# Kernel tuning notes

Hardware: AMD Instinct MI355X
Metric: run time of the kernel (lower is better)

## Reference

```python
import jax, jax.numpy as jnp
import numpy as np

IN_CH, OUT_CH, B, H, W = 32, 64, 8, 256, 256
EPS = 1e-5

SOBEL_X = [[1., 0., -1.], [2., 0., -2.], [1., 0., -1.]]
SOBEL_Y = [[1., 2., 1.], [0., 0., 0.], [-1., -2., -1.]]
LAP = [[0., 1., 0.], [1., -4., 1.], [0., 1., 0.]]

DN = ('NCHW', 'OIHW', 'NCHW')


def conv2d(x, w, b, pad, groups=1):
    y = jax.lax.conv_general_dilated(x, w, (1, 1), [(pad, pad), (pad, pad)],
                                     dimension_numbers=DN, feature_group_count=groups)
    return y + b[None, :, None, None]


def dw_conv(x, k2d):
    # fixed depthwise 3x3 conv, groups=C, padding=1, no bias
    c = x.shape[1]
    kern = jnp.tile(jnp.asarray(k2d, x.dtype)[None, None], (c, 1, 1, 1))  # (C,1,3,3)
    return jax.lax.conv_general_dilated(x, kern, (1, 1), [(1, 1), (1, 1)],
                                        dimension_numbers=DN, feature_group_count=c)


def bn4d(x, p):  # eval-mode BN; x (B,C,H,W), p (4,C) = gamma, beta, mean, var
    g, b, m, v = p
    s = g * jax.lax.rsqrt(v + EPS)
    return (x - m[None, :, None, None]) * s[None, :, None, None] + b[None, :, None, None]


def bn2d(h, p):  # h (B,C)
    g, b, m, v = p
    return (h - m) * (g * jax.lax.rsqrt(v + EPS)) + b


def _bn_params(key, c):
    k1, k2, k3, k4 = jax.random.split(key, 4)
    g = 1.0 + 0.1 * jax.random.normal(k1, (c,), jnp.float32)
    b = 0.1 * jax.random.normal(k2, (c,), jnp.float32)
    m = 0.1 * jax.random.normal(k3, (c,), jnp.float32)
    v = jax.random.uniform(k4, (c,), jnp.float32, 0.5, 1.5)
    return jnp.stack([g, b, m, v])


def setup_inputs() -> dict:
    key = jax.random.key(0)
    ks = jax.random.split(key, 24)
    s = 0.05
    return {
        'x': jax.random.normal(ks[0], (B, IN_CH, H, W), jnp.float32),
        'gate_w1': s * jax.random.normal(ks[1], (IN_CH, IN_CH), jnp.float32),
        'gate_b1': s * jax.random.normal(ks[2], (IN_CH,), jnp.float32),
        'gate_bn': _bn_params(ks[3], IN_CH),
        'gate_w2': s * jax.random.normal(ks[4], (3, IN_CH), jnp.float32),
        'gate_b2': s * jax.random.normal(ks[5], (3,), jnp.float32),
        'mw1': s * jax.random.normal(ks[6], (OUT_CH, IN_CH, 3, 3), jnp.float32),
        'mb1': s * jax.random.normal(ks[7], (OUT_CH,), jnp.float32),
        'mbn1': _bn_params(ks[8], OUT_CH),
        'mw2': s * jax.random.normal(ks[9], (OUT_CH, OUT_CH, 5, 5), jnp.float32),
        'mb2': s * jax.random.normal(ks[10], (OUT_CH,), jnp.float32),
        'mbn2': _bn_params(ks[11], OUT_CH),
        'sxw': s * jax.random.normal(ks[12], (OUT_CH, IN_CH, 5, 5), jnp.float32),
        'sxb': s * jax.random.normal(ks[13], (OUT_CH,), jnp.float32),
        'sxbn': _bn_params(ks[14], OUT_CH),
        'syw': s * jax.random.normal(ks[15], (OUT_CH, IN_CH, 5, 5), jnp.float32),
        'syb': s * jax.random.normal(ks[16], (OUT_CH,), jnp.float32),
        'sybn': _bn_params(ks[17], OUT_CH),
        'lw': s * jax.random.normal(ks[18], (OUT_CH, IN_CH, 5, 5), jnp.float32),
        'lb': s * jax.random.normal(ks[19], (OUT_CH,), jnp.float32),
        'lbn': _bn_params(ks[20], OUT_CH),
    }


def reference(x, gate_w1, gate_b1, gate_bn, gate_w2, gate_b2,
              mw1, mb1, mbn1, mw2, mb2, mbn2,
              sxw, sxb, sxbn, syw, syb, sybn, lw, lb, lbn):
    # gate: GAP -> 1x1 conv -> BN -> tanh -> 1x1 conv -> top-1 one-hot over 3 experts
    gap = x.mean((2, 3))                                   # (B, C_in)
    h = jnp.tanh(bn2d(gap @ gate_w1.T + gate_b1, gate_bn))
    k = h @ gate_w2.T + gate_b2                            # (B, 3)
    oh = jax.nn.one_hot(jnp.argmax(k, axis=1), 3, dtype=x.dtype)  # (B, 3)

    # expert 0: main branch (conv3x3+BN+ReLU -> conv5x5+BN+ReLU)
    main = jax.nn.relu(bn4d(conv2d(x, mw1, mb1, 1), mbn1))
    main = jax.nn.relu(bn4d(conv2d(main, mw2, mb2, 2), mbn2))

    # expert 1: mean of sobel-x and sobel-y branches
    sx = jax.nn.relu(bn4d(conv2d(dw_conv(x, SOBEL_X), sxw, sxb, 2), sxbn))
    sy = jax.nn.relu(bn4d(conv2d(dw_conv(x, SOBEL_Y), syw, syb, 2), sybn))
    sobel = (sx + sy) * 0.5

    # expert 2: laplacian branch
    lap = jax.nn.relu(bn4d(conv2d(dw_conv(x, LAP), lw, lb, 2), lbn))

    # one-hot gated combination (== stack + one_hot mask + sum in the original)
    w = oh[:, :, None, None, None]  # (B, 3, 1, 1, 1)
    return main * w[:, 0] + sobel * w[:, 1] + lap * w[:, 2]
```

## Files before the change

### kernel.cpp

```cpp
#include <hip/hip_runtime.h>

#define BB 8
#define IC 32
#define OC 64
#define HH 256
#define WW 256
#define EPS 1e-5f

typedef __attribute__((ext_vector_type(8))) short bf16x8;
typedef __attribute__((ext_vector_type(4))) float f32x4;

#define YSTR 40
#define XSTR 40

#define WS_GAP   0
#define WS_BIDX  256
#define WS_W1F   264
#define WS_B1F   (WS_W1F + 9216)
#define WS_W2F   (WS_B1F + 64)
#define WS_B2F   (WS_W2F + 51200)
#define WS_SXWT  (WS_B2F + 64)
#define WS_SXBF  (WS_SXWT + 51200)
#define WS_SYWT  (WS_SXBF + 64)
#define WS_SYBF  (WS_SYWT + 51200)
#define WS_LWT   (WS_SYBF + 64)
#define WS_LBF   (WS_LWT + 51200)
#define WS_XT    (WS_LBF + 64)
#define WS_ZPAD  (WS_XT + 8388608)
#define WS_NEED_FAST ((size_t)(WS_ZPAD + 16) * 4)

__device__ inline unsigned short bf16r(float f) {
    unsigned int u = __float_as_uint(f);
    unsigned int r = (u + 0x7fffu + ((u >> 16) & 1u)) >> 16;
    return (unsigned short)r;
}
__device__ inline float bf2f(unsigned short s) {
    return __uint_as_float(((unsigned int)s) << 16);
}

__device__ __forceinline__ void gld16(const void* g, const void* l) {
    __builtin_amdgcn_global_load_lds(
        (const __attribute__((address_space(1))) void*)(unsigned long long)(g),
        (__attribute__((address_space(3))) void*)(unsigned int)(unsigned long long)(l),
        16, 0, 0);
}

__global__ void prep_kernel(const float* __restrict__ mw1, const float* __restrict__ mb1, const float* __restrict__ mbn1,
                            const float* __restrict__ mw2, const float* __restrict__ mb2, const float* __restrict__ mbn2,
                            const float* __restrict__ sxw, const float* __restrict__ sxb, const float* __restrict__ sxbn,
                            const float* __restrict__ syw, const float* __restrict__ syb, const float* __restrict__ sybn,
                            const float* __restrict__ lw,  const float* __restrict__ lb,  const float* __restrict__ lbn,
                            float* __restrict__ ws, int fast) {
    int idx = blockIdx.x * 256 + threadIdx.x;

    if (idx < 18432) {
        int j = idx & 7, lane = (idx >> 3) & 63, oct = (idx >> 9) & 1, ht = idx >> 10;
        int t = ht % 9, h = ht / 9;
        int oc = h * 32 + oct * 16 + (lane & 15);
        int ic = (lane >> 4) * 8 + j;
        float s = mbn1[oc] * rsqrtf(mbn1[192 + oc] + EPS);
        ((unsigned short*)(ws + WS_W1F))[idx] = bf16r(mw1[(oc * IC + ic) * 9 + t] * s);
    }
    if (idx < 102400) {
        int j = idx & 7, lane = (idx >> 3) & 63, oct = (idx >> 9) & 3, ht = idx >> 11;
        int t = ht % 25, h = ht / 25;
        int oc = oct * 16 + (lane & 15);
        int ic = h * 32 + (lane >> 4) * 8 + j;
        float s = mbn2[oc] * rsqrtf(mbn2[192 + oc] + EPS);
        ((unsigned short*)(ws + WS_W2F))[idx] = bf16r(mw2[(oc * OC + ic) * 25 + t] * s);
    }
    if (idx < 51200) {
        int j = idx & 7, lane = (idx >> 3) & 63, oct = (idx >> 9) & 3, t = idx >> 11;
        int oc = oct * 16 + (lane & 15);
        int ic = (lane >> 4) * 8 + j;
        float ssx = sxbn[oc] * rsqrtf(sxbn[192 + oc] + EPS);
        float ssy = sybn[oc] * rsqrtf(sybn[192 + oc] + EPS);
        float sl  = lbn[oc]  * rsqrtf(lbn[192 + oc]  + EPS);
        ((unsigned short*)(ws + WS_SXWT))[idx] = bf16r(sxw[(oc * IC + ic) * 25 + t] * ssx);
        ((unsigned short*)(ws + WS_SYWT))[idx] = bf16r(syw[(oc * IC + ic) * 25 + t] * ssy);
        ((unsigned short*)(ws + WS_LWT ))[idx] = bf16r(lw [(oc * IC + ic) * 25 + t] * sl);
    }
    if (idx < 256) ws[WS_GAP + idx] = 0.f;
    if (fast && idx < 16) ws[WS_ZPAD + idx] = 0.f;
    if (idx < 64) {
        float s1 = mbn1[idx] * rsqrtf(mbn1[192 + idx] + EPS);
        ws[WS_B1F + idx] = (mb1[idx] - mbn1[128 + idx]) * s1 + mbn1[64 + idx];
        float s2 = mbn2[idx] * rsqrtf(mbn2[192 + idx] + EPS);
        ws[WS_B2F + idx] = (mb2[idx] - mbn2[128 + idx]) * s2 + mbn2[64 + idx];
        float sx = sxbn[idx] * rsqrtf(sxbn[192 + idx] + EPS);
        ws[WS_SXBF + idx] = (sxb[idx] - sxbn[128 + idx]) * sx + sxbn[64 + idx];
        float sy = sybn[idx] * rsqrtf(sybn[192 + idx] + EPS);
        ws[WS_SYBF + idx] = (syb[idx] - sybn[128 + idx]) * sy + sybn[64 + idx];
        float sl = lbn[idx] * rsqrtf(lbn[192 + idx] + EPS);
        ws[WS_LBF + idx] = (lb[idx] - lbn[128 + idx]) * sl + lbn[64 + idx];
    }
}

__global__ void __launch_bounds__(256, 2)
xform_kernel(const float* __restrict__ x, float* __restrict__ ws) {
    int b = blockIdx.y, row = blockIdx.x, t = threadIdx.x;
    const float* xb = x + (size_t)b * (IC * HH * WW) + (size_t)row * WW;

    unsigned int pk[16];
    #pragma unroll
    for (int k = 0; k < 32; k += 2) {
        float v0 = xb[(size_t)k * (HH * WW) + t];
        float v1 = xb[(size_t)(k + 1) * (HH * WW) + t];
        pk[k >> 1] = (unsigned int)bf16r(v0) | ((unsigned int)bf16r(v1) << 16);
    }
    short* xt = (short*)(ws + WS_XT) + ((size_t)b * (HH * WW) + (size_t)row * WW + t) * 32;
    uint4* dp = (uint4*)xt;
    dp[0] = make_uint4(pk[0],  pk[1],  pk[2],  pk[3]);
    dp[1] = make_uint4(pk[4],  pk[5],  pk[6],  pk[7]);
    dp[2] = make_uint4(pk[8],  pk[9],  pk[10], pk[11]);
    dp[3] = make_uint4(pk[12], pk[13], pk[14], pk[15]);

    __shared__ float gl[32];
    int w = t >> 6, lane = t & 63;
    #pragma unroll
    for (int kk = 0; kk < 8; kk++) {
        int k = w * 8 + kk;
        const float* rp = xb + (size_t)k * (HH * WW);
        float s = rp[lane] + rp[lane + 64] + rp[lane + 128] + rp[lane + 192];
        #pragma unroll
        for (int off = 32; off; off >>= 1) s += __shfl_down(s, off, 64);
        if (lane == 0) gl[k] = s;
    }
    __syncthreads();
    if (t < 32) atomicAdd(ws + WS_GAP + b * 32 + t, gl[t] * (1.f / (HH * WW)));
}

__global__ void gap_kernel(const float* __restrict__ x, float* __restrict__ ws) {
    int bc = blockIdx.x;
    const float4* p = (const float4*)(x + (size_t)bc * (HH * WW));
    float s = 0.f;
    for (int i = threadIdx.x; i < (HH * WW) / 4; i += 256) {
        float4 v = p[i];
        s += (v.x + v.y) + (v.z + v.w);
    }
    #pragma unroll
    for (int off = 32; off; off >>= 1) s += __shfl_down(s, off, 64);
    __shared__ float red[4];
    int lane = threadIdx.x & 63, w = threadIdx.x >> 6;
    if (lane == 0) red[w] = s;
    __syncthreads();
    if (threadIdx.x == 0)
        ws[WS_GAP + bc] = (red[0] + red[1] + red[2] + red[3]) * (1.f / (HH * WW));
}

__global__ void gate_kernel(const float* __restrict__ w1, const float* __restrict__ b1,
                            const float* __restrict__ gbn,
                            const float* __restrict__ w2, const float* __restrict__ b2,
                            float* __restrict__ ws) {
    __shared__ float hsh[8][32];
    int tid = threadIdx.x;
    int b = tid >> 5, j = tid & 31;
    float acc = b1[j];
    for (int i = 0; i < 32; i++) acc += ws[WS_GAP + b * 32 + i] * w1[j * 32 + i];
    float s = gbn[j] * rsqrtf(gbn[96 + j] + EPS);
    hsh[b][j] = tanhf((acc - gbn[64 + j]) * s + gbn[32 + j]);
    __syncthreads();
    if (tid < 8) {
        float best = -1e30f; int bi = 0;
        for (int c = 0; c < 3; c++) {
            float k = b2[c];
            for (int jj = 0; jj < 32; jj++) k += hsh[tid][jj] * w2[c * 32 + jj];
            if (k > best) { best = k; bi = c; }
        }
        ((int*)ws)[WS_BIDX + tid] = bi;
    }
}

template <int ASYNC>
__global__ void __launch_bounds__(256, 2)
main_kernel(const float* __restrict__ x, const float* __restrict__ ws, float* __restrict__ out) {
    __shared__ __align__(1024) short xs[ASYNC ? 496 * 32 : 484 * XSTR];
    __shared__ __align__(16)   short ys[400 * YSTR];

    int b = blockIdx.y;
    if (((const int*)ws)[WS_BIDX + b] != 0) return;
    int tile = blockIdx.x;
    int ty = (tile >> 4) * 16, tx = (tile & 15) * 16;
    int tid = threadIdx.x;
    int w = tid >> 6, lane = tid & 63, n = lane & 15, quad = lane >> 4;

    if constexpr (ASYNC) {
        const short* xtb = (const short*)(ws + WS_XT) + (size_t)b * (HH * WW * 32);
        const void* zp = (const void*)(ws + WS_ZPAD);
        for (int c = w; c < 31; c += 4) {
            int D = c * 1024 + (lane << 4);
            int L = D ^ (((D >> 7) & 7) << 4);
            int pL = L >> 6, qL = (L >> 4) & 3;
            int rr = pL / 22, cc2 = pL - rr * 22;
            int gy = ty - 3 + rr, gx = tx - 3 + cc2;
            bool v = (pL < 484) && ((unsigned)gy < HH) && ((unsigned)gx < WW);
            const void* src = v ? (const void*)(xtb + (((gy << 8) + gx) * 32) + (qL << 3)) : zp;
            gld16(src, (const void*)((const char*)xs + c * 1024));
        }
    } else {
        const float* xb = x + (size_t)b * IC * HH * WW;
        for (int p = tid; p < 484; p += 256) {
            int rr = p / 22, cc = p % 22;
            int gy = ty - 3 + rr, gx = tx - 3 + cc;
            bool v = ((unsigned)gy < HH) && ((unsigned)gx < WW);
            const float* xp = xb + gy * WW + gx;
            short* dst = xs + p * XSTR;
            #pragma unroll
            for (int ic = 0; ic < IC; ic += 4) {
                float f0 = v ? xp[(size_t)(ic + 0) * (HH * WW)] : 0.f;
                float f1 = v ? xp[(size_t)(ic + 1) * (HH * WW)] : 0.f;
                float f2 = v ? xp[(size_t)(ic + 2) * (HH * WW)] : 0.f;
                float f3 = v ? xp[(size_t)(ic + 3) * (HH * WW)] : 0.f;
                uint2 pk;
                pk.x = (unsigned int)bf16r(f0) | ((unsigned int)bf16r(f1) << 16);
                pk.y = (unsigned int)bf16r(f2) | ((unsigned int)bf16r(f3) << 16);
                *(uint2*)(dst + ic) = pk;
            }
        }
    }

    auto ldb = [&](int P) -> bf16x8 {
        if constexpr (ASYNC) {
            int L = (P << 6) + (quad << 4);
            int A = L ^ (((L >> 7) & 7) << 4);
            return *(const bf16x8*)((const char*)xs + A);
        } else {
            return *(const bf16x8*)(xs + P * XSTR + quad * 8);
        }
    };

    const short* w1v = (const short*)(ws + WS_W1F);
    const bf16x8* w2v = (const bf16x8*)(ws + WS_W2F);

    f32x4 acc2[4][4];
    #pragma unroll
    for (int i = 0; i < 4; i++)
        #pragma unroll
        for (int jj = 0; jj < 4; jj++) acc2[i][jj] = (f32x4){0.f, 0.f, 0.f, 0.f};
    int mrow0 = w * 4;
    int yr0   = w * 5;

    __syncthreads();

    #pragma unroll 1
    for (int h = 0; h < 2; h++) {
        if (h) __syncthreads();

        #pragma unroll
        for (int cg = 0; cg < 2; cg++) {
            int cb = cg * 4;
            f32x4 a1[5][2];
            #pragma unroll
            for (int rr = 0; rr < 5; rr++) {
                a1[rr][0] = (f32x4){0.f, 0.f, 0.f, 0.f};
                a1[rr][1] = (f32x4){0.f, 0.f, 0.f, 0.f};
            }
            #pragma unroll
            for (int dw = 0; dw < 3; dw++) {
                bf16x8 w1f[3][2];
                #pragma unroll
                for (int dh = 0; dh < 3; dh++) {
                    int t = dh * 3 + dw;
                    w1f[dh][0] = *(const bf16x8*)(w1v + (((h * 9 + t) * 2 + 0) * 64 + lane) * 8);
                    w1f[dh][1] = *(const bf16x8*)(w1v + (((h * 9 + t) * 2 + 1) * 64 + lane) * 8);
                }
                bf16x8 bfr[7];
                #pragma unroll
                for (int rI = 0; rI < 7; rI++)
                    bfr[rI] = ldb((yr0 + rI) * 22 + cb + n + dw);
                #pragma unroll
                for (int dh = 0; dh < 3; dh++)
                    #pragma unroll
                    for (int rr = 0; rr < 5; rr++) {
                        a1[rr][0] = __builtin_amdgcn_mfma_f32_16x16x32_bf16(w1f[dh][0], bfr[rr + dh], a1[rr][0], 0, 0, 0);
                        a1[rr][1] = __builtin_amdgcn_mfma_f32_16x16x32_bf16(w1f[dh][1], bfr[rr + dh], a1[rr][1], 0, 0, 0);
                    }
            }
            #pragma unroll
            for (int oct = 0; oct < 2; oct++) {
                float bias1[4];
                #pragma unroll
                for (int r = 0; r < 4; r++)
                    bias1[r] = ws[WS_B1F + h * 32 + oct * 16 + quad * 4 + r];
                #pragma unroll
                for (int rr = 0; rr < 5; rr++) {
                    int yr = yr0 + rr;
                    int gy2 = ty - 2 + yr, gx2 = tx - 2 + cb + n;
                    bool inb = ((unsigned)gy2 < HH) && ((unsigned)gx2 < WW);
                    float v0 = inb ? fmaxf(a1[rr][oct][0] + bias1[0], 0.f) : 0.f;
                    float v1 = inb ? fmaxf(a1[rr][oct][1] + bias1[1], 0.f) : 0.f;
                    float v2 = inb ? fmaxf(a1[rr][oct][2] + bias1[2], 0.f) : 0.f;
                    float v3 = inb ? fmaxf(a1[rr][oct][3] + bias1[3], 0.f) : 0.f;
                    uint2 pkk;
                    pkk.x = (unsigned int)bf16r(v0) | ((unsigned int)bf16r(v1) << 16);
                    pkk.y = (unsigned int)bf16r(v2) | ((unsigned int)bf16r(v3) << 16);
                    *(uint2*)(ys + (yr * 20 + cb + n) * YSTR + oct * 16 + quad * 4) = pkk;
                }
            }
        }
        __syncthreads();

        const bf16x8* w2h = w2v + (size_t)h * 100 * 64;
        bf16x8 afq[4][4];
        #pragma unroll
        for (int kp = 0; kp < 4; kp++) {
            int tn = (kp % 5) * 5 + (kp / 5);
            int base = tn * 256 + lane;
            afq[kp][0] = w2h[base];       afq[kp][1] = w2h[base + 64];
            afq[kp][2] = w2h[base + 128]; afq[kp][3] = w2h[base + 192];
        }
        bf16x8 bfr2[8];
        #pragma unroll
        for (int k = 0; k < 25; k++) {
            int dw = k / 5, dh = k % 5;
            if (dh == 0) {
                #pragma unroll
                for (int rI = 0; rI < 8; rI++)
                    bfr2[rI] = *(const bf16x8*)(ys + ((mrow0 + rI) * 20 + n + dw) * YSTR + quad * 8);
            }
            #pragma unroll
            for (int r4 = 0; r4 < 4; r4++) {
                bf16x8 bb = bfr2[r4 + dh];
                acc2[r4][0] = __builtin_amdgcn_mfma_f32_16x16x32_bf16(afq[k & 3][0], bb, acc2[r4][0], 0, 0, 0);
                acc2[r4][1] = __builtin_amdgcn_mfma_f32_16x16x32_bf16(afq[k & 3][1], bb, acc2[r4][1], 0, 0, 0);
                acc2[r4][2] = __builtin_amdgcn_mfma_f32_16x16x32_bf16(afq[k & 3][2], bb, acc2[r4][2], 0, 0, 0);
                acc2[r4][3] = __builtin_amdgcn_mfma_f32_16x16x32_bf16(afq[k & 3][3], bb, acc2[r4][3], 0, 0, 0);
            }
            if (k + 4 < 25) {
                int kk = k + 4;
                int tn = (kk % 5) * 5 + (kk / 5);
                int base = tn * 256 + lane;
                afq[k & 3][0] = w2h[base];       afq[k & 3][1] = w2h[base + 64];
                afq[k & 3][2] = w2h[base + 128]; afq[k & 3][3] = w2h[base + 192];
            }
        }
    }

    float bias2[4][4];
    #pragma unroll
    for (int oct = 0; oct < 4; oct++)
        #pragma unroll
        for (int r = 0; r < 4; r++)
            bias2[oct][r] = ws[WS_B2F + oct * 16 + quad * 4 + r];

    float* ob = out + (size_t)b * OC * HH * WW;
    #pragma unroll
    for (int r4 = 0; r4 < 4; r4++) {
        int orow = mrow0 + r4;
        #pragma unroll
        for (int oct = 0; oct < 4; oct++) {
            #pragma unroll
            for (int r = 0; r < 4; r++) {
                int oc = oct * 16 + quad * 4 + r;
                float v = fmaxf(acc2[r4][oct][r] + bias2[oct][r], 0.f);
                ob[(size_t)oc * (HH * WW) + (ty + orow) * WW + tx + n] = v;
            }
        }
    }
}

template <int ASYNC>
__global__ void __launch_bounds__(256, 2)
edge_kernel(const float* __restrict__ x, const float* __restrict__ ws, float* __restrict__ out) {
    constexpr float KSX[9] = {1, 0, -1, 2, 0, -2, 1, 0, -1};
    constexpr float KSY[9] = {1, 2, 1, 0, 0, 0, -1, -2, -1};
    constexpr float KLP[9] = {0, 1, 0, 1, -4, 1, 0, 1, 0};

    __shared__ __align__(1024) short xs[ASYNC ? 496 * 32 : 484 * XSTR];
    __shared__ __align__(16)   short ys[400 * YSTR];

    int b = blockIdx.y;
    int sel = ((const int*)ws)[WS_BIDX + b];
    if (sel == 0) return;
    int tile = blockIdx.x;
    int ty = (tile >> 4) * 16, tx = (tile & 15) * 16;
    int tid = threadIdx.x;
    int w = tid >> 6, lane = tid & 63, n = lane & 15, quad = lane >> 4;

    if constexpr (ASYNC) {
        const short* xtb = (const short*)(ws + WS_XT) + (size_t)b * (HH * WW * 32);
        const void* zp = (const void*)(ws + WS_ZPAD);
        for (int c = w; c < 31; c += 4) {
            int D = c * 1024 + (lane << 4);
            int L = D ^ (((D >> 7) & 7) << 4);
            int pL = L >> 6, qL = (L >> 4) & 3;
            int rr = pL / 22, cc2 = pL - rr * 22;
            int gy = ty - 3 + rr, gx = tx - 3 + cc2;
            bool v = (pL < 484) && ((unsigned)gy < HH) && ((unsigned)gx < WW);
            const void* src = v ? (const void*)(xtb + (((gy << 8) + gx) * 32) + (qL << 3)) : zp;
            gld16(src, (const void*)((const char*)xs + c * 1024));
        }
    } else {
        const float* xb = x + (size_t)b * IC * HH * WW;
        for (int p = tid; p < 484; p += 256) {
            int rr = p / 22, cc = p % 22;
            int gy = ty - 3 + rr, gx = tx - 3 + cc;
            bool v = ((unsigned)gy < HH) && ((unsigned)gx < WW);
            const float* xp = xb + gy * WW + gx;
            short* dst = xs + p * XSTR;
            #pragma unroll
            for (int ic = 0; ic < IC; ic += 4) {
                float f0 = v ? xp[(size_t)(ic + 0) * (HH * WW)] : 0.f;
                float f1 = v ? xp[(size_t)(ic + 1) * (HH * WW)] : 0.f;
                float f2 = v ? xp[(size_t)(ic + 2) * (HH * WW)] : 0.f;
                float f3 = v ? xp[(size_t)(ic + 3) * (HH * WW)] : 0.f;
                uint2 pk;
                pk.x = (unsigned int)bf16r(f0) | ((unsigned int)bf16r(f1) << 16);
                pk.y = (unsigned int)bf16r(f2) | ((unsigned int)bf16r(f3) << 16);
                *(uint2*)(dst + ic) = pk;
            }
        }
    }

    auto ldq = [&](int P, int q) -> bf16x8 {
        if constexpr (ASYNC) {
            int L = (P << 6) + (q << 4);
            int A = L ^ (((L >> 7) & 7) << 4);
            return *(const bf16x8*)((const char*)xs + A);
        } else {
            return *(const bf16x8*)(xs + P * XSTR + q * 8);
        }
    };

    int mrow0 = w * 4;
    int npass = (sel == 1) ? 2 : 1;
    f32x4 accA[4][4];
    f32x4 acc2[4][4];

    __syncthreads();

    #pragma unroll 1
    for (int pass = 0; pass < npass; pass++) {
        int kid = (sel == 1) ? pass : 2;
        if (pass) __syncthreads();

        for (int t2 = tid; t2 < 1600; t2 += 256) {
            int q = t2 & 3, px = t2 >> 2;
            int pr = px / 20, pc = px - pr * 20;
            bool inb = ((unsigned)(ty - 2 + pr) < HH) && ((unsigned)(tx - 2 + pc) < WW);
            float a[8] = {0.f, 0.f, 0.f, 0.f, 0.f, 0.f, 0.f, 0.f};
            if (inb) {
                #pragma unroll
                for (int dr = 0; dr < 3; dr++)
                    #pragma unroll
                    for (int dc = 0; dc < 3; dc++) {
                        float kv = (kid == 0) ? KSX[dr * 3 + dc]
                                 : (kid == 1) ? KSY[dr * 3 + dc]
                                              : KLP[dr * 3 + dc];
                        if (kv != 0.f) {
                            bf16x8 v = ldq((pr + dr) * 22 + pc + dc, q);
                            #pragma unroll
                            for (int j = 0; j < 8; j++)
                                a[j] += kv * bf2f((unsigned short)v[j]);
                        }
                    }
            }
            uint4 pk;
            pk.x = (unsigned int)bf16r(a[0]) | ((unsigned int)bf16r(a[1]) << 16);
            pk.y = (unsigned int)bf16r(a[2]) | ((unsigned int)bf16r(a[3]) << 16);
            pk.z = (unsigned int)bf16r(a[4]) | ((unsigned int)bf16r(a[5]) << 16);
            pk.w = (unsigned int)bf16r(a[6]) | ((unsigned int)bf16r(a[7]) << 16);
            *(uint4*)(ys + px * YSTR + q * 8) = pk;
        }
        __syncthreads();

        #pragma unroll
        for (int i = 0; i < 4; i++)
            #pragma unroll
            for (int jj = 0; jj < 4; jj++) acc2[i][jj] = (f32x4){0.f, 0.f, 0.f, 0.f};

        const bf16x8* wf = (const bf16x8*)(ws + (kid == 0 ? WS_SXWT : kid == 1 ? WS_SYWT : WS_LWT));
        bf16x8 afq[2][4];
        #pragma unroll
        for (int kp = 0; kp < 2; kp++) {
            int tn = kp * 5;
            int base = tn * 256 + lane;
            afq[kp][0] = wf[base];       afq[kp][1] = wf[base + 64];
            afq[kp][2] = wf[base + 128]; afq[kp][3] = wf[base + 192];
        }
        bf16x8 bfr2[8];
        #pragma unroll
        for (int k = 0; k < 25; k++) {
            int dw = k / 5, dh = k % 5;
            if (dh == 0) {
                #pragma unroll
                for (int rI = 0; rI < 8; rI++)
                    bfr2[rI] = *(const bf16x8*)(ys + ((mrow0 + rI) * 20 + n + dw) * YSTR + quad * 8);
            }
            #pragma unroll
            for (int r4 = 0; r4 < 4; r4++) {
                bf16x8 bb = bfr2[r4 + dh];
                acc2[r4][0] = __builtin_amdgcn_mfma_f32_16x16x32_bf16(afq[k & 1][0], bb, acc2[r4][0], 0, 0, 0);
                acc2[r4][1] = __builtin_amdgcn_mfma_f32_16x16x32_bf16(afq[k & 1][1], bb, acc2[r4][1], 0, 0, 0);
                acc2[r4][2] = __builtin_amdgcn_mfma_f32_16x16x32_bf16(afq[k & 1][2], bb, acc2[r4][2], 0, 0, 0);
                acc2[r4][3] = __builtin_amdgcn_mfma_f32_16x16x32_bf16(afq[k & 1][3], bb, acc2[r4][3], 0, 0, 0);
            }
            if (k + 2 < 25) {
                int kk = k + 2;
                int tn = (kk % 5) * 5 + (kk / 5);
                int base = tn * 256 + lane;
                afq[k & 1][0] = wf[base];       afq[k & 1][1] = wf[base + 64];
                afq[k & 1][2] = wf[base + 128]; afq[k & 1][3] = wf[base + 192];
            }
        }
        if (sel == 1 && pass == 0) {
            #pragma unroll
            for (int i = 0; i < 4; i++)
                #pragma unroll
                for (int jj = 0; jj < 4; jj++) accA[i][jj] = acc2[i][jj];
        }
    }

    float* ob = out + (size_t)b * OC * HH * WW;
    #pragma unroll
    for (int r4 = 0; r4 < 4; r4++) {
        int orow = mrow0 + r4;
        #pragma unroll
        for (int oct = 0; oct < 4; oct++) {
            #pragma unroll
            for (int r = 0; r < 4; r++) {
                int oc = oct * 16 + quad * 4 + r;
                float v;
                if (sel == 1) {
                    float vx = fmaxf(accA[r4][oct][r] + ws[WS_SXBF + oc], 0.f);
                    float vy = fmaxf(acc2[r4][oct][r] + ws[WS_SYBF + oc], 0.f);
                    v = 0.5f * (vx + vy);
                } else {
                    v = fmaxf(acc2[r4][oct][r] + ws[WS_LBF + oc], 0.f);
                }
                ob[(size_t)oc * (HH * WW) + (ty + orow) * WW + tx + n] = v;
            }
        }
    }
}

extern "C" void kernel_launch(void* const* d_in, const int* in_sizes, int n_in,
                              void* d_out, int out_size, void* d_ws, size_t ws_size,
                              hipStream_t stream) {
    const float* x    = (const float*)d_in[0];
    const float* gw1  = (const float*)d_in[1];
    const float* gb1  = (const float*)d_in[2];
    const float* gbn  = (const float*)d_in[3];
    const float* gw2  = (const float*)d_in[4];
    const float* gb2  = (const float*)d_in[5];
    const float* mw1  = (const float*)d_in[6];
    const float* mb1  = (const float*)d_in[7];
    const float* mbn1 = (const float*)d_in[8];
    const float* mw2  = (const float*)d_in[9];
    const float* mb2  = (const float*)d_in[10];
    const float* mbn2 = (const float*)d_in[11];
    const float* sxw  = (const float*)d_in[12];
    const float* sxb  = (const float*)d_in[13];
    const float* sxbn = (const float*)d_in[14];
    const float* syw  = (const float*)d_in[15];
    const float* syb  = (const float*)d_in[16];
    const float* sybn = (const float*)d_in[17];
    const float* lw   = (const float*)d_in[18];
    const float* lb   = (const float*)d_in[19];
    const float* lbn  = (const float*)d_in[20];
    float* ws  = (float*)d_ws;
    float* out = (float*)d_out;

    int fast = (ws_size >= WS_NEED_FAST) ? 1 : 0;

    prep_kernel<<<400, 256, 0, stream>>>(mw1, mb1, mbn1, mw2, mb2, mbn2,
                                         sxw, sxb, sxbn, syw, syb, sybn, lw, lb, lbn, ws, fast);
    if (fast) {
        xform_kernel<<<dim3(HH, BB), 256, 0, stream>>>(x, ws);
    } else {
        gap_kernel<<<256, 256, 0, stream>>>(x, ws);
    }
    gate_kernel<<<1, 256, 0, stream>>>(gw1, gb1, gbn, gw2, gb2, ws);

    dim3 grid(256, BB);
    if (fast) {
        main_kernel<1><<<grid, 256, 0, stream>>>(x, ws, out);
        edge_kernel<1><<<grid, 256, 0, stream>>>(x, ws, out);
    } else {
        main_kernel<0><<<grid, 256, 0, stream>>>(x, ws, out);
        edge_kernel<0><<<grid, 256, 0, stream>>>(x, ws, out);
    }
}
```

Baseline: 435.7 us.

## Pad transformed input with zero halo and read main-branch operands directly from global

```diff
diff --git a/kernel.cpp b/kernel.cpp
--- a/kernel.cpp
+++ b/kernel.cpp
@@ -6,6 +6,9 @@
 #define HH 256
 #define WW 256
 #define EPS 1e-5f
+
+#define XTW 264
+#define XTP (XTW * XTW)
 
 typedef __attribute__((ext_vector_type(8))) short bf16x8;
 typedef __attribute__((ext_vector_type(4))) float f32x4;
@@ -26,7 +29,8 @@
 #define WS_LWT   (WS_SYBF + 64)
 #define WS_LBF   (WS_LWT + 51200)
 #define WS_XT    (WS_LBF + 64)
-#define WS_ZPAD  (WS_XT + 8388608)
+#define WS_XT_U4 2230272
+#define WS_ZPAD  (WS_XT + 8921088)
 #define WS_NEED_FAST ((size_t)(WS_ZPAD + 16) * 4)
 
 __device__ inline unsigned short bf16r(float f) {
@@ -52,6 +56,9 @@
                             const float* __restrict__ lw,  const float* __restrict__ lb,  const float* __restrict__ lbn,
                             float* __restrict__ ws, int fast) {
     int idx = blockIdx.x * 256 + threadIdx.x;
+
+    if (fast && idx < WS_XT_U4)
+        ((uint4*)(ws + WS_XT))[idx] = make_uint4(0u, 0u, 0u, 0u);
 
     if (idx < 18432) {
         int j = idx & 7, lane = (idx >> 3) & 63, oct = (idx >> 9) & 1, ht = idx >> 10;
@@ -108,7 +115,7 @@
         float v1 = xb[(size_t)(k + 1) * (HH * WW) + t];
         pk[k >> 1] = (unsigned int)bf16r(v0) | ((unsigned int)bf16r(v1) << 16);
     }
-    short* xt = (short*)(ws + WS_XT) + ((size_t)b * (HH * WW) + (size_t)row * WW + t) * 32;
+    short* xt = (short*)(ws + WS_XT) + ((size_t)b * XTP + (size_t)(row + 3) * XTW + (t + 3)) * 32;
     uint4* dp = (uint4*)xt;
     dp[0] = make_uint4(pk[0],  pk[1],  pk[2],  pk[3]);
     dp[1] = make_uint4(pk[4],  pk[5],  pk[6],  pk[7]);
@@ -172,10 +179,10 @@
 }
 
 template <int ASYNC>
-__global__ void __launch_bounds__(256, 2)
+__global__ void __launch_bounds__(256, ASYNC ? 4 : 2)
 main_kernel(const float* __restrict__ x, const float* __restrict__ ws, float* __restrict__ out) {
-    __shared__ __align__(1024) short xs[ASYNC ? 496 * 32 : 484 * XSTR];
-    __shared__ __align__(16)   short ys[400 * YSTR];
+    __shared__ __align__(16) short xs[ASYNC ? 8 : 484 * XSTR];
+    __shared__ __align__(16) short ys[400 * YSTR];
 
     int b = blockIdx.y;
     if (((const int*)ws)[WS_BIDX + b] != 0) return;
@@ -184,19 +191,9 @@
     int tid = threadIdx.x;
     int w = tid >> 6, lane = tid & 63, n = lane & 15, quad = lane >> 4;
 
+    const short* xtb = nullptr;
     if constexpr (ASYNC) {
-        const short* xtb = (const short*)(ws + WS_XT) + (size_t)b * (HH * WW * 32);
-        const void* zp = (const void*)(ws + WS_ZPAD);
-        for (int c = w; c < 31; c += 4) {
-            int D = c * 1024 + (lane << 4);
-            int L = D ^ (((D >> 7) & 7) << 4);
-            int pL = L >> 6, qL = (L >> 4) & 3;
-            int rr = pL / 22, cc2 = pL - rr * 22;
-            int gy = ty - 3 + rr, gx = tx - 3 + cc2;
-            bool v = (pL < 484) && ((unsigned)gy < HH) && ((unsigned)gx < WW);
-            const void* src = v ? (const void*)(xtb + (((gy << 8) + gx) * 32) + (qL << 3)) : zp;
-            gld16(src, (const void*)((const char*)xs + c * 1024));
-        }
+        xtb = (const short*)(ws + WS_XT) + (size_t)b * (XTP * 32);
     } else {
         const float* xb = x + (size_t)b * IC * HH * WW;
         for (int p = tid; p < 484; p += 256) {
@@ -219,13 +216,11 @@
         }
     }
 
-    auto ldb = [&](int P) -> bf16x8 {
+    auto ldb = [&](int row, int col) -> bf16x8 {
         if constexpr (ASYNC) {
-            int L = (P << 6) + (quad << 4);
-            int A = L ^ (((L >> 7) & 7) << 4);
-            return *(const bf16x8*)((const char*)xs + A);
+            return *(const bf16x8*)(xtb + ((size_t)((ty + row) * XTW + tx + col)) * 32 + quad * 8);
         } else {
-            return *(const bf16x8*)(xs + P * XSTR + quad * 8);
+            return *(const bf16x8*)(xs + (row * 22 + col) * XSTR + quad * 8);
         }
     };
 
@@ -240,7 +235,7 @@
     int mrow0 = w * 4;
     int yr0   = w * 5;
 
-    __syncthreads();
+    if constexpr (!ASYNC) __syncthreads();
 
     #pragma unroll 1
     for (int h = 0; h < 2; h++) {
@@ -267,7 +262,7 @@
                 bf16x8 bfr[7];
                 #pragma unroll
                 for (int rI = 0; rI < 7; rI++)
-                    bfr[rI] = ldb((yr0 + rI) * 22 + cb + n + dw);
+                    bfr[rI] = ldb(yr0 + rI, cb + n + dw);
                 #pragma unroll
                 for (int dh = 0; dh < 3; dh++)
                     #pragma unroll
@@ -378,16 +373,15 @@
     int w = tid >> 6, lane = tid & 63, n = lane & 15, quad = lane >> 4;
 
     if constexpr (ASYNC) {
-        const short* xtb = (const short*)(ws + WS_XT) + (size_t)b * (HH * WW * 32);
+        const short* xtb = (const short*)(ws + WS_XT) + (size_t)b * (XTP * 32);
         const void* zp = (const void*)(ws + WS_ZPAD);
         for (int c = w; c < 31; c += 4) {
             int D = c * 1024 + (lane << 4);
             int L = D ^ (((D >> 7) & 7) << 4);
             int pL = L >> 6, qL = (L >> 4) & 3;
             int rr = pL / 22, cc2 = pL - rr * 22;
-            int gy = ty - 3 + rr, gx = tx - 3 + cc2;
-            bool v = (pL < 484) && ((unsigned)gy < HH) && ((unsigned)gx < WW);
-            const void* src = v ? (const void*)(xtb + (((gy << 8) + gx) * 32) + (qL << 3)) : zp;
+            bool v = (pL < 484);
+            const void* src = v ? (const void*)(xtb + ((size_t)((ty + rr) * XTW + tx + cc2)) * 32 + (qL << 3)) : zp;
             gld16(src, (const void*)((const char*)xs + c * 1024));
         }
     } else {
@@ -563,8 +557,9 @@
 
     int fast = (ws_size >= WS_NEED_FAST) ? 1 : 0;
 
-    prep_kernel<<<400, 256, 0, stream>>>(mw1, mb1, mbn1, mw2, mb2, mbn2,
-                                         sxw, sxb, sxbn, syw, syb, sybn, lw, lb, lbn, ws, fast);
+    prep_kernel<<<fast ? (WS_XT_U4 / 256) : 400, 256, 0, stream>>>(
+        mw1, mb1, mbn1, mw2, mb2, mbn2,
+        sxw, sxb, sxbn, syw, syb, sybn, lw, lb, lbn, ws, fast);
     if (fast) {
         xform_kernel<<<dim3(HH, BB), 256, 0, stream>>>(x, ws);
     } else {
```

Result: slower. 874.9 us (+100.8%).
